# Optimization experiments

Measured on AMD Instinct MI355X. Metric: run time of the kernel, lower is better.

Reference implementation:

```python
import jax, jax.numpy as jnp
import numpy as np

D_K = 64
N_HEADS = 16
D_MODEL = 1024
EPS = 1e-5


def setup_inputs() -> dict:
    key = jax.random.key(0)
    ks = jax.random.split(key, 8)
    B, S = 2, 2048
    scale = 1.0 / np.sqrt(D_MODEL)
    inp = {
        "input_Q": jax.random.normal(ks[0], (B, S, D_MODEL), jnp.float32),
        "input_K": jax.random.normal(ks[1], (B, S, D_MODEL), jnp.float32),
        "input_V": jax.random.normal(ks[2], (B, S, D_MODEL), jnp.float32),
        "attn_mask": jax.random.randint(ks[3], (B, S, S), 0, 2) == 1,
        "W_Q": jax.random.normal(ks[4], (D_MODEL, N_HEADS * D_K), jnp.float32) * scale,
        "W_K": jax.random.normal(ks[5], (D_MODEL, N_HEADS * D_K), jnp.float32) * scale,
        "W_V": jax.random.normal(ks[6], (D_MODEL, N_HEADS * D_K), jnp.float32) * scale,
        "W_fc": jax.random.normal(ks[7], (N_HEADS * D_K, D_MODEL), jnp.float32) * scale,
    }
    return inp


def _layer_norm(x):
    mu = jnp.mean(x, axis=-1, keepdims=True)
    var = jnp.var(x, axis=-1, keepdims=True)
    return (x - mu) / jnp.sqrt(var + EPS)


def reference(input_Q, input_K, input_V, attn_mask, W_Q, W_K, W_V, W_fc):
    B, S, _ = input_Q.shape
    # projections -> [B, H, S, d_k]
    Q = (input_Q @ W_Q).reshape(B, S, N_HEADS, D_K).transpose(0, 2, 1, 3)
    K = (input_K @ W_K).reshape(B, S, N_HEADS, D_K).transpose(0, 2, 1, 3)
    V = (input_V @ W_V).reshape(B, S, N_HEADS, D_K).transpose(0, 2, 1, 3)
    scores = jnp.einsum("bhqd,bhkd->bhqk", Q, K) / np.sqrt(D_K)
    scores = jnp.where(attn_mask[:, None, :, :], -1e9, scores)
    attn = jax.nn.softmax(scores, axis=-1)
    context = jnp.einsum("bhqk,bhkd->bhqd", attn, V)
    context = context.transpose(0, 2, 1, 3).reshape(B, S, N_HEADS * D_K)
    output = context @ W_fc
    return _layer_norm(output + input_Q), attn
```

## Files before the change

kernel.cpp:

```cpp
#include <hip/hip_runtime.h>

typedef __bf16 bf16x8 __attribute__((ext_vector_type(8)));
typedef unsigned short u16x8 __attribute__((ext_vector_type(8)));
typedef unsigned short u16x4 __attribute__((ext_vector_type(4)));
typedef float f32x4 __attribute__((ext_vector_type(4)));

#define DEV static __device__ __forceinline__

DEV unsigned short f2bf(float f) {
  union { float f; unsigned u; } v; v.f = f;
  unsigned u = v.u + 0x7FFFu + ((v.u >> 16) & 1u);
  return (unsigned short)(u >> 16);
}

DEV float bf2f(unsigned short b) {
  union { unsigned u; float f; } v; v.u = ((unsigned)b) << 16;
  return v.f;
}

DEV float fast_exp2(float x) { return __builtin_amdgcn_exp2f(x); }

DEV int swz(int row, int k) { return row * 64 + (k ^ ((row & 7) * 8)); }

#define GLOAD16(gp, lp)                                                        \
  __builtin_amdgcn_global_load_lds(                                            \
      (const __attribute__((address_space(1))) void*)(const void*)(gp),        \
      (__attribute__((address_space(3))) void*)(void*)(lp), 16, 0, 0)

__global__ __launch_bounds__(256) void k_detect(const unsigned* m, int* flag) {
  __shared__ int sF, sI;
  if (threadIdx.x == 0) { sF = 1; sI = 1; }
  __syncthreads();
  int lF = 1, lI = 1;
  for (int i = threadIdx.x; i < 4096; i += 256) {
    unsigned d = m[i];
    lF &= (d == 0u || d == 0x3F800000u);
    lI &= (d == 0u || d == 1u);
  }
  if (!lF) atomicAnd(&sF, 0);
  if (!lI) atomicAnd(&sI, 0);
  __syncthreads();
  if (threadIdx.x == 0) flag[0] = sF ? 2 : (sI ? 0 : 1);
}

__global__ __launch_bounds__(256) void k_pack(const void* m, const int* flag,
                                              unsigned long long* bits) {
  const int tid = threadIdx.x;
  const int w = blockIdx.x * 4 + (tid >> 6);
  const int lane = tid & 63;
  const size_t idx = (size_t)w * 64 + lane;
  const int fl = flag[0];
  int v;
  if (fl == 1)      v = ((const unsigned char*)m)[idx];
  else if (fl == 0) v = ((const int*)m)[idx];
  else              v = (((const float*)m)[idx] != 0.f);
  unsigned long long bal = __ballot(v != 0);
  if (lane == 0) bits[w] = bal;
}

__global__ __launch_bounds__(256) void k_cvt(const float* a, const float* b,
                                             const float* c, unsigned short* out) {
  const int gid = blockIdx.x * 256 + threadIdx.x;
  const int which = gid >> 20;
  const int loc = gid & 1048575;
  const float* src = which == 0 ? a : which == 1 ? b : c;
  float4 f = ((const float4*)src)[loc];
  ushort4 u = make_ushort4(f2bf(f.x), f2bf(f.y), f2bf(f.z), f2bf(f.w));
  *(ushort4*)(out + (size_t)which * 4194304 + (size_t)loc * 4) = u;
}

__global__ __launch_bounds__(256) void k_wt(const float* w0, const float* w1,
                                            const float* w2, const float* w3,
                                            unsigned short* out) {
  __shared__ float t[32][33];
  const int z = blockIdx.z;
  const float* W = z == 0 ? w0 : z == 1 ? w1 : z == 2 ? w2 : w3;
  unsigned short* Wt = out + (size_t)z * 1048576;
  const int x = threadIdx.x, y = threadIdx.y;
  const int k0 = blockIdx.x * 32, n0 = blockIdx.y * 32;
#pragma unroll
  for (int r = 0; r < 4; ++r)
    t[y + r * 8][x] = W[(size_t)(k0 + y + r * 8) * 1024 + n0 + x];
  __syncthreads();
#pragma unroll
  for (int r = 0; r < 4; ++r)
    Wt[(size_t)(n0 + y + r * 8) * 1024 + k0 + x] = f2bf(t[x][y + r * 8]);
}

__global__ __launch_bounds__(256) void k_gemm(
    const unsigned short* __restrict__ A0, const unsigned short* __restrict__ A1,
    const unsigned short* __restrict__ A2, const unsigned short* __restrict__ B0,
    const unsigned short* __restrict__ B1, const unsigned short* __restrict__ B2,
    unsigned short* __restrict__ C0, unsigned short* __restrict__ C1,
    unsigned short* __restrict__ C2, float* __restrict__ Cf) {
  __shared__ __align__(16) unsigned short As[128 * 64];
  __shared__ __align__(16) unsigned short Bs[128 * 64];
  const int z = blockIdx.z;
  const unsigned short* A = z == 0 ? A0 : z == 1 ? A1 : A2;
  const unsigned short* Bt = z == 0 ? B0 : z == 1 ? B1 : B2;
  unsigned short* Cb = z == 0 ? C0 : z == 1 ? C1 : C2;

  const int tid = threadIdx.x, lane = tid & 63, wid = tid >> 6;
  const int mt = blockIdx.x, nt = blockIdx.y;
  const int wm = (wid >> 1) * 64, wn = (wid & 1) * 64;
  const int lr = lane >> 3;
  const int lc = ((lane & 7) ^ (lane >> 3)) * 8;
  const int l15 = lane & 15, lg = lane >> 4;
  f32x4 acc[4][4] = {};

  for (int kt = 0; kt < 16; ++kt) {
    const int k0 = kt * 64;
#pragma unroll
    for (int c = wid; c < 16; c += 4) {
      GLOAD16(A + (size_t)(mt * 128 + c * 8 + lr) * 1024 + k0 + lc, As + c * 512);
      GLOAD16(Bt + (size_t)(nt * 128 + c * 8 + lr) * 1024 + k0 + lc, Bs + c * 512);
    }
    __syncthreads();
#pragma unroll
    for (int ks = 0; ks < 2; ++ks) {
      const int ko = ks * 32 + lg * 8;
      bf16x8 af[4], bfr[4];
#pragma unroll
      for (int f = 0; f < 4; ++f) {
        af[f] = *(const bf16x8*)(As + swz(wm + f * 16 + l15, ko));
        bfr[f] = *(const bf16x8*)(Bs + swz(wn + f * 16 + l15, ko));
      }
#pragma unroll
      for (int i = 0; i < 4; ++i)
#pragma unroll
        for (int j = 0; j < 4; ++j)
          acc[i][j] = __builtin_amdgcn_mfma_f32_16x16x32_bf16(af[i], bfr[j],
                                                              acc[i][j], 0, 0, 0);
    }
    __syncthreads();
  }
  const int rbase = mt * 128 + wm + lg * 4;
  const int cbase = nt * 128 + wn + l15;
#pragma unroll
  for (int i = 0; i < 4; ++i)
#pragma unroll
    for (int j = 0; j < 4; ++j) {
      const int col = cbase + j * 16;
#pragma unroll
      for (int r = 0; r < 4; ++r) {
        const int row = rbase + i * 16 + r;
        if (Cf) Cf[(size_t)row * 1024 + col] = acc[i][j][r];
        else    Cb[(size_t)row * 1024 + col] = f2bf(acc[i][j][r]);
      }
    }
}

__global__ __launch_bounds__(256) void k_attn(
    const unsigned short* __restrict__ PQ, const unsigned short* __restrict__ PK,
    const unsigned short* __restrict__ PV_, const unsigned long long* __restrict__ bits,
    float* __restrict__ attn_out, unsigned short* __restrict__ CTX) {
  __shared__ __align__(16) unsigned short KB[2][64 * 64];
  __shared__ __align__(16) unsigned short VB[2][64 * 64];
  __shared__ __align__(16) unsigned short Ps[4][16 * 64];

  const int tid = threadIdx.x, lane = tid & 63, wid = tid >> 6;
  const int qt = blockIdx.x, h = blockIdx.y, b = blockIdx.z;
  const int q0 = qt * 64;
  const int lr = lane >> 3;
  const int lc = ((lane & 7) ^ (lane >> 3)) * 8;
  const int l15 = lane & 15, lg = lane >> 4;
  const size_t rowK = (size_t)(b * 2048) * 1024 + h * 64;
  const float C = 0.125f * 1.44269504f;

#pragma unroll
  for (int c = wid; c < 8; c += 4)
    GLOAD16(PQ + rowK + (size_t)(q0 + c * 8 + lr) * 1024 + lc, KB[0] + c * 512);
  __syncthreads();
  const bf16x8 qf0 = *(const bf16x8*)(KB[0] + swz(wid * 16 + l15, lg * 8));
  const bf16x8 qf1 = *(const bf16x8*)(KB[0] + swz(wid * 16 + l15, 32 + lg * 8));
  const unsigned long long* mrow =
      bits + (size_t)(b * 2048 + q0 + wid * 16 + lg * 4) * 32;
  __syncthreads();

#pragma unroll
  for (int c = wid; c < 8; c += 4)
    GLOAD16(PK + rowK + (size_t)(c * 8 + lr) * 1024 + lc, KB[0] + c * 512);
  __syncthreads();

  float rs[4] = {0.f, 0.f, 0.f, 0.f};
  int cur = 0;
  for (int kt = 0; kt < 32; ++kt) {
    if (kt < 31) {
#pragma unroll
      for (int c = wid; c < 8; c += 4)
        GLOAD16(PK + rowK + (size_t)((kt + 1) * 64 + c * 8 + lr) * 1024 + lc,
                KB[cur ^ 1] + c * 512);
    }
    const unsigned long long w0 = mrow[kt], w1 = mrow[32 + kt],
                             w2 = mrow[64 + kt], w3 = mrow[96 + kt];
#pragma unroll
    for (int fn = 0; fn < 4; ++fn) {
      const bf16x8 kf0 = *(const bf16x8*)(KB[cur] + swz(fn * 16 + l15, lg * 8));
      const bf16x8 kf1 = *(const bf16x8*)(KB[cur] + swz(fn * 16 + l15, 32 + lg * 8));
      f32x4 s = {};
      s = __builtin_amdgcn_mfma_f32_16x16x32_bf16(qf0, kf0, s, 0, 0, 0);
      s = __builtin_amdgcn_mfma_f32_16x16x32_bf16(qf1, kf1, s, 0, 0, 0);
      const int kb = fn * 16 + l15;
      rs[0] += ((w0 >> kb) & 1) ? 0.f : fast_exp2(s[0] * C);
      rs[1] += ((w1 >> kb) & 1) ? 0.f : fast_exp2(s[1] * C);
      rs[2] += ((w2 >> kb) & 1) ? 0.f : fast_exp2(s[2] * C);
      rs[3] += ((w3 >> kb) & 1) ? 0.f : fast_exp2(s[3] * C);
    }
    __syncthreads();
    cur ^= 1;
  }
#pragma unroll
  for (int r = 0; r < 4; ++r) {
#pragma unroll
    for (int m = 1; m < 16; m <<= 1) rs[r] += __shfl_xor(rs[r], m);
    rs[r] = 1.f / rs[r];
  }

  const int vr = tid >> 3, d0 = (tid & 7) * 8;
  {
#pragma unroll
    for (int c = wid; c < 8; c += 4)
      GLOAD16(PK + rowK + (size_t)(c * 8 + lr) * 1024 + lc, KB[0] + c * 512);
    u16x8 v0 = *(const u16x8*)(PV_ + rowK + (size_t)vr * 1024 + d0);
    u16x8 v1 = *(const u16x8*)(PV_ + rowK + (size_t)(32 + vr) * 1024 + d0);
#pragma unroll
    for (int e = 0; e < 8; ++e) VB[0][swz(d0 + e, vr)] = v0[e];
#pragma unroll
    for (int e = 0; e < 8; ++e) VB[0][swz(d0 + e, 32 + vr)] = v1[e];
    __syncthreads();
  }

  f32x4 cacc[4] = {};
  cur = 0;
  const int srow = lane >> 2, scg = lane & 3;
  float* arow = attn_out + ((size_t)(b * 16 + h) * 2048 + q0 + wid * 16 + srow) * 2048;
  for (int kt = 0; kt < 32; ++kt) {
    const int k0 = kt * 64;
    u16x8 nv0, nv1;
    if (kt < 31) {
      const size_t nb = rowK + (size_t)((kt + 1) * 64) * 1024;
      nv0 = *(const u16x8*)(PV_ + nb + (size_t)vr * 1024 + d0);
      nv1 = *(const u16x8*)(PV_ + nb + (size_t)(32 + vr) * 1024 + d0);
#pragma unroll
      for (int c = wid; c < 8; c += 4)
        GLOAD16(PK + nb + (size_t)(c * 8 + lr) * 1024 + lc, KB[cur ^ 1] + c * 512);
    }
    const unsigned long long wm_[4] = {mrow[kt], mrow[32 + kt], mrow[64 + kt],
                                       mrow[96 + kt]};
#pragma unroll
    for (int fn = 0; fn < 4; ++fn) {
      const bf16x8 kf0 = *(const bf16x8*)(KB[cur] + swz(fn * 16 + l15, lg * 8));
      const bf16x8 kf1 = *(const bf16x8*)(KB[cur] + swz(fn * 16 + l15, 32 + lg * 8));
      f32x4 s = {};
      s = __builtin_amdgcn_mfma_f32_16x16x32_bf16(qf0, kf0, s, 0, 0, 0);
      s = __builtin_amdgcn_mfma_f32_16x16x32_bf16(qf1, kf1, s, 0, 0, 0);
      const int kb = fn * 16 + l15;
#pragma unroll
      for (int r = 0; r < 4; ++r) {
        const float p =
            ((wm_[r] >> kb) & 1) ? 0.f : fast_exp2(s[r] * C) * rs[r];
        Ps[wid][swz(lg * 4 + r, kb)] = f2bf(p);
      }
    }
#pragma unroll
    for (int j = 0; j < 4; ++j) {
      const int c = scg * 4 + j * 16;
      const u16x4 pb = *(const u16x4*)(&Ps[wid][swz(srow, c)]);
      float4 o;
      o.x = bf2f(pb[0]); o.y = bf2f(pb[1]); o.z = bf2f(pb[2]); o.w = bf2f(pb[3]);
      *(float4*)(arow + k0 + c) = o;
    }
#pragma unroll
    for (int ks = 0; ks < 2; ++ks) {
      const int ko = ks * 32 + lg * 8;
      const bf16x8 pf = *(const bf16x8*)(&Ps[wid][swz(l15, ko)]);
#pragma unroll
      for (int fn = 0; fn < 4; ++fn) {
        const bf16x8 vf = *(const bf16x8*)(VB[cur] + swz(fn * 16 + l15, ko));
        cacc[fn] = __builtin_amdgcn_mfma_f32_16x16x32_bf16(pf, vf, cacc[fn], 0, 0, 0);
      }
    }
    if (kt < 31) {
#pragma unroll
      for (int e = 0; e < 8; ++e) VB[cur ^ 1][swz(d0 + e, vr)] = nv0[e];
#pragma unroll
      for (int e = 0; e < 8; ++e) VB[cur ^ 1][swz(d0 + e, 32 + vr)] = nv1[e];
    }
    __syncthreads();
    cur ^= 1;
  }
#pragma unroll
  for (int fn = 0; fn < 4; ++fn)
#pragma unroll
    for (int r = 0; r < 4; ++r) {
      const int q = q0 + wid * 16 + lg * 4 + r;
      CTX[(size_t)(b * 2048 + q) * 1024 + h * 64 + fn * 16 + l15] =
          f2bf(cacc[fn][r]);
    }
}

__global__ __launch_bounds__(256) void k_ln(const float* __restrict__ PRE,
                                            const float* __restrict__ inQ,
                                            float* __restrict__ out) {
  const int row = blockIdx.x, tid = threadIdx.x;
  const size_t base = (size_t)row * 1024 + tid * 4;
  const float4 x = *(const float4*)(PRE + base);
  const float4 q = *(const float4*)(inQ + base);
  const float v0 = x.x + q.x, v1 = x.y + q.y, v2 = x.z + q.z, v3 = x.w + q.w;
  float s = v0 + v1 + v2 + v3;
  float ss = v0 * v0 + v1 * v1 + v2 * v2 + v3 * v3;
#pragma unroll
  for (int m = 1; m < 64; m <<= 1) {
    s += __shfl_xor(s, m);
    ss += __shfl_xor(ss, m);
  }
  __shared__ float red[8];
  const int wid = tid >> 6, lane = tid & 63;
  if (lane == 0) { red[wid] = s; red[4 + wid] = ss; }
  __syncthreads();
  if (tid == 0) {
    const float S = red[0] + red[1] + red[2] + red[3];
    const float SS = red[4] + red[5] + red[6] + red[7];
    const float mu = S * (1.f / 1024.f);
    const float var = SS * (1.f / 1024.f) - mu * mu;
    red[0] = mu;
    red[1] = rsqrtf(var + 1e-5f);
  }
  __syncthreads();
  const float mu = red[0], rstd = red[1];
  float4 o;
  o.x = (v0 - mu) * rstd; o.y = (v1 - mu) * rstd;
  o.z = (v2 - mu) * rstd; o.w = (v3 - mu) * rstd;
  *(float4*)(out + base) = o;
}

extern "C" void kernel_launch(void* const* d_in, const int* in_sizes, int n_in,
                              void* d_out, int out_size, void* d_ws, size_t ws_size,
                              hipStream_t stream) {
  const float* inQ = (const float*)d_in[0];
  const float* inK = (const float*)d_in[1];
  const float* inV = (const float*)d_in[2];
  const void* msk = d_in[3];
  const float* wq = (const float*)d_in[4];
  const float* wk = (const float*)d_in[5];
  const float* wv = (const float*)d_in[6];
  const float* wf = (const float*)d_in[7];

  char* ws = (char*)d_ws;
  unsigned short* XQ = (unsigned short*)(ws);
  unsigned short* WT = (unsigned short*)(ws + 25165824);
  unsigned short* PQ = (unsigned short*)(ws + 33554432);
  unsigned short* PK = (unsigned short*)(ws + 41943040);
  unsigned short* PV = (unsigned short*)(ws + 50331648);
  unsigned short* CTX = (unsigned short*)(ws + 58720256);
  float* PRE = (float*)(ws + 67108864);
  unsigned long long* BITS = (unsigned long long*)(ws + 83886080);
  int* FLAG = (int*)(ws + 84934656);

  float* outLN = (float*)d_out;
  float* outAT = (float*)d_out + 4194304;

  k_detect<<<1, 256, 0, stream>>>((const unsigned*)msk, FLAG);
  k_pack<<<32768, 256, 0, stream>>>(msk, FLAG, BITS);
  k_cvt<<<12288, 256, 0, stream>>>(inQ, inK, inV, XQ);
  k_wt<<<dim3(32, 32, 4), dim3(32, 8, 1), 0, stream>>>(wq, wk, wv, wf, WT);
  k_gemm<<<dim3(32, 8, 3), 256, 0, stream>>>(XQ, XQ + 4194304, XQ + 8388608,
                                             WT, WT + 1048576, WT + 2097152,
                                             PQ, PK, PV, nullptr);
  k_attn<<<dim3(32, 16, 2), 256, 0, stream>>>(PQ, PK, PV, BITS, outAT, CTX);
  k_gemm<<<dim3(32, 8, 1), 256, 0, stream>>>(CTX, CTX, CTX, WT + 3145728,
                                             WT + 3145728, WT + 3145728,
                                             nullptr, nullptr, nullptr, PRE);
  k_ln<<<4096, 256, 0, stream>>>(PRE, inQ, outLN);
}
```

Baseline: 396.9 us.

## Split attention into context kernel and probability-output kernel with bf16 additive mask

Replaces the packed bit mask with a bf16 additive mask buffer (0 or -1e30) and splits the two-pass attention kernel into two kernels. The first computes unnormalized P·V along with the row sums and rescales the context at the end. The second recomputes the scores and writes the normalized attention matrix. This removes the serial dependency between the row-sum pass and the PV pass, but the mask traffic grows sixteenfold (8 MB of bits becomes 16 MB of bf16, read per element by every head) and QK^T is still computed twice. The mask buffer MF also aliases PRE in the workspace, which is safe only because PRE is written after both attention kernels finish.

```diff
diff --git a/kernel.cpp b/kernel.cpp
--- a/kernel.cpp
+++ b/kernel.cpp
@@ -43,19 +43,15 @@
   if (threadIdx.x == 0) flag[0] = sF ? 2 : (sI ? 0 : 1);
 }
 
-__global__ __launch_bounds__(256) void k_pack(const void* m, const int* flag,
-                                              unsigned long long* bits) {
-  const int tid = threadIdx.x;
-  const int w = blockIdx.x * 4 + (tid >> 6);
-  const int lane = tid & 63;
-  const size_t idx = (size_t)w * 64 + lane;
+__global__ __launch_bounds__(256) void k_maskf(const void* m, const int* flag,
+                                               unsigned short* MF) {
+  const size_t idx = (size_t)blockIdx.x * 256 + threadIdx.x;
   const int fl = flag[0];
   int v;
   if (fl == 1)      v = ((const unsigned char*)m)[idx];
   else if (fl == 0) v = ((const int*)m)[idx];
   else              v = (((const float*)m)[idx] != 0.f);
-  unsigned long long bal = __ballot(v != 0);
-  if (lane == 0) bits[w] = bal;
+  MF[idx] = v ? f2bf(-1e30f) : (unsigned short)0;
 }
 
 __global__ __launch_bounds__(256) void k_cvt(const float* a, const float* b,
@@ -150,10 +146,10 @@
     }
 }
 
-__global__ __launch_bounds__(256) void k_attn(
+__global__ __launch_bounds__(256) void k_attnA(
     const unsigned short* __restrict__ PQ, const unsigned short* __restrict__ PK,
-    const unsigned short* __restrict__ PV_, const unsigned long long* __restrict__ bits,
-    float* __restrict__ attn_out, unsigned short* __restrict__ CTX) {
+    const unsigned short* __restrict__ PV_, const unsigned short* __restrict__ MF,
+    float* __restrict__ RS, unsigned short* __restrict__ CTX) {
   __shared__ __align__(16) unsigned short KB[2][64 * 64];
   __shared__ __align__(16) unsigned short VB[2][64 * 64];
   __shared__ __align__(16) unsigned short Ps[4][16 * 64];
@@ -173,26 +169,37 @@
   __syncthreads();
   const bf16x8 qf0 = *(const bf16x8*)(KB[0] + swz(wid * 16 + l15, lg * 8));
   const bf16x8 qf1 = *(const bf16x8*)(KB[0] + swz(wid * 16 + l15, 32 + lg * 8));
-  const unsigned long long* mrow =
-      bits + (size_t)(b * 2048 + q0 + wid * 16 + lg * 4) * 32;
-  __syncthreads();
-
-#pragma unroll
-  for (int c = wid; c < 8; c += 4)
-    GLOAD16(PK + rowK + (size_t)(c * 8 + lr) * 1024 + lc, KB[0] + c * 512);
-  __syncthreads();
+  const unsigned short* mrow =
+      MF + (size_t)(b * 2048 + q0 + wid * 16 + lg * 4) * 2048;
+  __syncthreads();
+
+  const int vr = tid >> 3, d0 = (tid & 7) * 8;
+  {
+#pragma unroll
+    for (int c = wid; c < 8; c += 4)
+      GLOAD16(PK + rowK + (size_t)(c * 8 + lr) * 1024 + lc, KB[0] + c * 512);
+    u16x8 v0 = *(const u16x8*)(PV_ + rowK + (size_t)vr * 1024 + d0);
+    u16x8 v1 = *(const u16x8*)(PV_ + rowK + (size_t)(32 + vr) * 1024 + d0);
+#pragma unroll
+    for (int e = 0; e < 8; ++e) VB[0][swz(d0 + e, vr)] = v0[e];
+#pragma unroll
+    for (int e = 0; e < 8; ++e) VB[0][swz(d0 + e, 32 + vr)] = v1[e];
+    __syncthreads();
+  }
 
   float rs[4] = {0.f, 0.f, 0.f, 0.f};
+  f32x4 cacc[4] = {};
   int cur = 0;
   for (int kt = 0; kt < 32; ++kt) {
+    u16x8 nv0, nv1;
     if (kt < 31) {
+      const size_t nb = rowK + (size_t)((kt + 1) * 64) * 1024;
+      nv0 = *(const u16x8*)(PV_ + nb + (size_t)vr * 1024 + d0);
+      nv1 = *(const u16x8*)(PV_ + nb + (size_t)(32 + vr) * 1024 + d0);
 #pragma unroll
       for (int c = wid; c < 8; c += 4)
-        GLOAD16(PK + rowK + (size_t)((kt + 1) * 64 + c * 8 + lr) * 1024 + lc,
-                KB[cur ^ 1] + c * 512);
-    }
-    const unsigned long long w0 = mrow[kt], w1 = mrow[32 + kt],
-                             w2 = mrow[64 + kt], w3 = mrow[96 + kt];
+        GLOAD16(PK + nb + (size_t)(c * 8 + lr) * 1024 + lc, KB[cur ^ 1] + c * 512);
+    }
 #pragma unroll
     for (int fn = 0; fn < 4; ++fn) {
       const bf16x8 kf0 = *(const bf16x8*)(KB[cur] + swz(fn * 16 + l15, lg * 8));
@@ -201,52 +208,102 @@
       s = __builtin_amdgcn_mfma_f32_16x16x32_bf16(qf0, kf0, s, 0, 0, 0);
       s = __builtin_amdgcn_mfma_f32_16x16x32_bf16(qf1, kf1, s, 0, 0, 0);
       const int kb = fn * 16 + l15;
-      rs[0] += ((w0 >> kb) & 1) ? 0.f : fast_exp2(s[0] * C);
-      rs[1] += ((w1 >> kb) & 1) ? 0.f : fast_exp2(s[1] * C);
-      rs[2] += ((w2 >> kb) & 1) ? 0.f : fast_exp2(s[2] * C);
-      rs[3] += ((w3 >> kb) & 1) ? 0.f : fast_exp2(s[3] * C);
+      const unsigned short* mc = mrow + kt * 64 + kb;
+#pragma unroll
+      for (int r = 0; r < 4; ++r) {
+        const float mval = bf2f(mc[(size_t)r * 2048]);
+        const float p = fast_exp2(__builtin_fmaf(s[r], C, mval));
+        rs[r] += p;
+        Ps[wid][swz(lg * 4 + r, kb)] = f2bf(p);
+      }
+    }
+#pragma unroll
+    for (int ks = 0; ks < 2; ++ks) {
+      const int ko = ks * 32 + lg * 8;
+      const bf16x8 pf = *(const bf16x8*)(&Ps[wid][swz(l15, ko)]);
+#pragma unroll
+      for (int fn = 0; fn < 4; ++fn) {
+        const bf16x8 vf = *(const bf16x8*)(VB[cur] + swz(fn * 16 + l15, ko));
+        cacc[fn] = __builtin_amdgcn_mfma_f32_16x16x32_bf16(pf, vf, cacc[fn], 0, 0, 0);
+      }
+    }
+    if (kt < 31) {
+#pragma unroll
+      for (int e = 0; e < 8; ++e) VB[cur ^ 1][swz(d0 + e, vr)] = nv0[e];
+#pragma unroll
+      for (int e = 0; e < 8; ++e) VB[cur ^ 1][swz(d0 + e, 32 + vr)] = nv1[e];
     }
     __syncthreads();
     cur ^= 1;
   }
+  float rsr[4];
 #pragma unroll
   for (int r = 0; r < 4; ++r) {
 #pragma unroll
     for (int m = 1; m < 16; m <<= 1) rs[r] += __shfl_xor(rs[r], m);
-    rs[r] = 1.f / rs[r];
-  }
-
-  const int vr = tid >> 3, d0 = (tid & 7) * 8;
-  {
-#pragma unroll
-    for (int c = wid; c < 8; c += 4)
-      GLOAD16(PK + rowK + (size_t)(c * 8 + lr) * 1024 + lc, KB[0] + c * 512);
-    u16x8 v0 = *(const u16x8*)(PV_ + rowK + (size_t)vr * 1024 + d0);
-    u16x8 v1 = *(const u16x8*)(PV_ + rowK + (size_t)(32 + vr) * 1024 + d0);
-#pragma unroll
-    for (int e = 0; e < 8; ++e) VB[0][swz(d0 + e, vr)] = v0[e];
-#pragma unroll
-    for (int e = 0; e < 8; ++e) VB[0][swz(d0 + e, 32 + vr)] = v1[e];
-    __syncthreads();
-  }
-
-  f32x4 cacc[4] = {};
-  cur = 0;
+    rsr[r] = 1.f / rs[r];
+  }
+#pragma unroll
+  for (int fn = 0; fn < 4; ++fn)
+#pragma unroll
+    for (int r = 0; r < 4; ++r) {
+      const int q = q0 + wid * 16 + lg * 4 + r;
+      CTX[(size_t)(b * 2048 + q) * 1024 + h * 64 + fn * 16 + l15] =
+          f2bf(cacc[fn][r] * rsr[r]);
+    }
+  if (l15 == 0) {
+#pragma unroll
+    for (int r = 0; r < 4; ++r)
+      RS[(size_t)(b * 16 + h) * 2048 + q0 + wid * 16 + lg * 4 + r] = rsr[r];
+  }
+}
+
+__global__ __launch_bounds__(256) void k_attnB(
+    const unsigned short* __restrict__ PQ, const unsigned short* __restrict__ PK,
+    const unsigned short* __restrict__ MF, const float* __restrict__ RS,
+    float* __restrict__ attn_out) {
+  __shared__ __align__(16) unsigned short KB[2][64 * 64];
+  __shared__ __align__(16) unsigned short Ps[4][16 * 64];
+
+  const int tid = threadIdx.x, lane = tid & 63, wid = tid >> 6;
+  const int qt = blockIdx.x, h = blockIdx.y, b = blockIdx.z;
+  const int q0 = qt * 64;
+  const int lr = lane >> 3;
+  const int lc = ((lane & 7) ^ (lane >> 3)) * 8;
+  const int l15 = lane & 15, lg = lane >> 4;
+  const size_t rowK = (size_t)(b * 2048) * 1024 + h * 64;
+  const float C = 0.125f * 1.44269504f;
+
+#pragma unroll
+  for (int c = wid; c < 8; c += 4)
+    GLOAD16(PQ + rowK + (size_t)(q0 + c * 8 + lr) * 1024 + lc, KB[0] + c * 512);
+  __syncthreads();
+  const bf16x8 qf0 = *(const bf16x8*)(KB[0] + swz(wid * 16 + l15, lg * 8));
+  const bf16x8 qf1 = *(const bf16x8*)(KB[0] + swz(wid * 16 + l15, 32 + lg * 8));
+  const unsigned short* mrow =
+      MF + (size_t)(b * 2048 + q0 + wid * 16 + lg * 4) * 2048;
+  float rsr[4];
+#pragma unroll
+  for (int r = 0; r < 4; ++r)
+    rsr[r] = RS[(size_t)(b * 16 + h) * 2048 + q0 + wid * 16 + lg * 4 + r];
+  __syncthreads();
+
+#pragma unroll
+  for (int c = wid; c < 8; c += 4)
+    GLOAD16(PK + rowK + (size_t)(c * 8 + lr) * 1024 + lc, KB[0] + c * 512);
+  __syncthreads();
+
   const int srow = lane >> 2, scg = lane & 3;
   float* arow = attn_out + ((size_t)(b * 16 + h) * 2048 + q0 + wid * 16 + srow) * 2048;
+  int cur = 0;
   for (int kt = 0; kt < 32; ++kt) {
     const int k0 = kt * 64;
-    u16x8 nv0, nv1;
     if (kt < 31) {
-      const size_t nb = rowK + (size_t)((kt + 1) * 64) * 1024;
-      nv0 = *(const u16x8*)(PV_ + nb + (size_t)vr * 1024 + d0);
-      nv1 = *(const u16x8*)(PV_ + nb + (size_t)(32 + vr) * 1024 + d0);
 #pragma unroll
       for (int c = wid; c < 8; c += 4)
-        GLOAD16(PK + nb + (size_t)(c * 8 + lr) * 1024 + lc, KB[cur ^ 1] + c * 512);
-    }
-    const unsigned long long wm_[4] = {mrow[kt], mrow[32 + kt], mrow[64 + kt],
-                                       mrow[96 + kt]};
+        GLOAD16(PK + rowK + (size_t)((kt + 1) * 64 + c * 8 + lr) * 1024 + lc,
+                KB[cur ^ 1] + c * 512);
+    }
 #pragma unroll
     for (int fn = 0; fn < 4; ++fn) {
       const bf16x8 kf0 = *(const bf16x8*)(KB[cur] + swz(fn * 16 + l15, lg * 8));
@@ -255,10 +312,11 @@
       s = __builtin_amdgcn_mfma_f32_16x16x32_bf16(qf0, kf0, s, 0, 0, 0);
       s = __builtin_amdgcn_mfma_f32_16x16x32_bf16(qf1, kf1, s, 0, 0, 0);
       const int kb = fn * 16 + l15;
+      const unsigned short* mc = mrow + kt * 64 + kb;
 #pragma unroll
       for (int r = 0; r < 4; ++r) {
-        const float p =
-            ((wm_[r] >> kb) & 1) ? 0.f : fast_exp2(s[r] * C) * rs[r];
+        const float mval = bf2f(mc[(size_t)r * 2048]);
+        const float p = fast_exp2(__builtin_fmaf(s[r], C, mval)) * rsr[r];
         Ps[wid][swz(lg * 4 + r, kb)] = f2bf(p);
       }
     }
@@ -270,33 +328,9 @@
       o.x = bf2f(pb[0]); o.y = bf2f(pb[1]); o.z = bf2f(pb[2]); o.w = bf2f(pb[3]);
       *(float4*)(arow + k0 + c) = o;
     }
-#pragma unroll
-    for (int ks = 0; ks < 2; ++ks) {
-      const int ko = ks * 32 + lg * 8;
-      const bf16x8 pf = *(const bf16x8*)(&Ps[wid][swz(l15, ko)]);
-#pragma unroll
-      for (int fn = 0; fn < 4; ++fn) {
-        const bf16x8 vf = *(const bf16x8*)(VB[cur] + swz(fn * 16 + l15, ko));
-        cacc[fn] = __builtin_amdgcn_mfma_f32_16x16x32_bf16(pf, vf, cacc[fn], 0, 0, 0);
-      }
-    }
-    if (kt < 31) {
-#pragma unroll
-      for (int e = 0; e < 8; ++e) VB[cur ^ 1][swz(d0 + e, vr)] = nv0[e];
-#pragma unroll
-      for (int e = 0; e < 8; ++e) VB[cur ^ 1][swz(d0 + e, 32 + vr)] = nv1[e];
-    }
     __syncthreads();
     cur ^= 1;
   }
-#pragma unroll
-  for (int fn = 0; fn < 4; ++fn)
-#pragma unroll
-    for (int r = 0; r < 4; ++r) {
-      const int q = q0 + wid * 16 + lg * 4 + r;
-      CTX[(size_t)(b * 2048 + q) * 1024 + h * 64 + fn * 16 + l15] =
-          f2bf(cacc[fn][r]);
-    }
 }
 
 __global__ __launch_bounds__(256) void k_ln(const float* __restrict__ PRE,
@@ -353,21 +387,23 @@
   unsigned short* PK = (unsigned short*)(ws + 41943040);
   unsigned short* PV = (unsigned short*)(ws + 50331648);
   unsigned short* CTX = (unsigned short*)(ws + 58720256);
+  unsigned short* MF = (unsigned short*)(ws + 67108864);
   float* PRE = (float*)(ws + 67108864);
-  unsigned long long* BITS = (unsigned long long*)(ws + 83886080);
-  int* FLAG = (int*)(ws + 84934656);
+  float* RS = (float*)(ws + 83886080);
+  int* FLAG = (int*)(ws + 84148224);
 
   float* outLN = (float*)d_out;
   float* outAT = (float*)d_out + 4194304;
 
   k_detect<<<1, 256, 0, stream>>>((const unsigned*)msk, FLAG);
-  k_pack<<<32768, 256, 0, stream>>>(msk, FLAG, BITS);
+  k_maskf<<<32768, 256, 0, stream>>>(msk, FLAG, MF);
   k_cvt<<<12288, 256, 0, stream>>>(inQ, inK, inV, XQ);
   k_wt<<<dim3(32, 32, 4), dim3(32, 8, 1), 0, stream>>>(wq, wk, wv, wf, WT);
   k_gemm<<<dim3(32, 8, 3), 256, 0, stream>>>(XQ, XQ + 4194304, XQ + 8388608,
                                              WT, WT + 1048576, WT + 2097152,
                                              PQ, PK, PV, nullptr);
-  k_attn<<<dim3(32, 16, 2), 256, 0, stream>>>(PQ, PK, PV, BITS, outAT, CTX);
+  k_attnA<<<dim3(32, 16, 2), 256, 0, stream>>>(PQ, PK, PV, MF, RS, CTX);
+  k_attnB<<<dim3(32, 16, 2), 256, 0, stream>>>(PQ, PK, MF, RS, outAT);
   k_gemm<<<dim3(32, 8, 1), 256, 0, stream>>>(CTX, CTX, CTX, WT + 3145728,
                                              WT + 3145728, WT + 3145728,
                                              nullptr, nullptr, nullptr, PRE);
```

New measurement: 415.2 us. 1.05x slower.
